# Performance work log

Hardware: AMD Instinct MI355X
Metric: run time of the kernel (lower is better)

The kernel has to match this reference:

```python
import jax, jax.numpy as jnp
import numpy as np

B, C, H, W = 16, 64, 64, 64

def setup_inputs() -> dict:
    key = jax.random.key(0)
    k1, k2, k3, k4, k5 = jax.random.split(key, 5)
    x = jax.random.normal(k1, (B, C, H, W), dtype=jnp.float32)
    w1 = jax.random.normal(k2, (C // 2, C), dtype=jnp.float32) * (1.0 / np.sqrt(C))
    w2 = jax.random.normal(k3, (C // 2, C), dtype=jnp.float32) * (1.0 / np.sqrt(C))
    w3 = jax.random.normal(k4, (C, C), dtype=jnp.float32) * (1.0 / np.sqrt(C))
    gamma = jax.random.normal(k5, (1,), dtype=jnp.float32)
    return {"x": x, "w1": w1, "w2": w2, "w3": w3, "gamma": gamma}

def reference(x, w1, w2, w3, gamma):
    b, c, h, w = x.shape
    n = h * w
    xf = x.reshape(b, c, n)                      # [B, C, N] (1x1 conv == channel matmul)
    c1 = jnp.einsum('dc,bcn->bdn', w1, xf)       # [B, C/2, N]
    c2 = jnp.einsum('dc,bcn->bdn', w2, xf)       # [B, C/2, N]
    c3 = jnp.einsum('oc,bcn->bon', w3, xf)       # [B, C, N]
    # matrix[b,i,j] = sum_d c2[b,d,i] * c1[b,d,j]
    matrix = jnp.einsum('bdi,bdj->bij', c2, c1)  # [B, N, N]
    attention = jax.nn.softmax(matrix, axis=-1)  # softmax over last dim
    # refined[b,c,k] = sum_j c3[b,c,j] * attention[b,k,j]
    refined = jnp.einsum('bcj,bkj->bck', c3, attention)  # [B, C, N]
    refined = refined.reshape(b, c, h, w)
    return gamma[0] * refined + x
```

## Files before the change

kernel.cpp:

```cpp
#include <hip/hip_runtime.h>
#include <hip/hip_bf16.h>

#define Bn 16
#define Nn 4096

typedef __attribute__((ext_vector_type(8))) short bf16x8;
typedef __attribute__((ext_vector_type(16))) float f32x16;

static __device__ __forceinline__ unsigned short f2bf(float f) {
    union { float f; unsigned int u; } v; v.f = f;
    return (unsigned short)((v.u + 0x7fffu + ((v.u >> 16) & 1u)) >> 16);
}
static __device__ __forceinline__ int cvtpk(float lo, float hi) {
    int d; asm("v_cvt_pk_bf16_f32 %0, %1, %2" : "=v"(d) : "v"(lo), "v"(hi)); return d;
}
static __device__ __forceinline__ bf16x8 mkfrag(int a, int b, int c, int d) {
    union { int i[4]; bf16x8 v; } u; u.i[0]=a; u.i[1]=b; u.i[2]=c; u.i[3]=d; return u.v;
}

__global__ __launch_bounds__(256) void qkv_kernel(
    const float* __restrict__ x,
    const float* __restrict__ w1,
    const float* __restrict__ w2,
    const float* __restrict__ w3,
    uint4* __restrict__ Qf,
    uint4* __restrict__ Kf,
    uint4* __restrict__ Vf)
{
    __shared__ float wlds[128 * 64];
    __shared__ __align__(16) unsigned short vtile[64][136];

    const int t = threadIdx.x;
    {
        float4* wd = (float4*)wlds;
        const float4* s1 = (const float4*)w1;
        const float4* s2 = (const float4*)w2;
        const float4* s3 = (const float4*)w3;
        wd[t]       = s1[t];
        wd[256 + t] = s1[256 + t];
        wd[512 + t] = s2[t];
        wd[768 + t] = s2[256 + t];
        #pragma unroll
        for (int k = 0; k < 4; ++k) wd[1024 + k * 256 + t] = s3[k * 256 + t];
    }

    const int half = t >> 7;
    const int nl = t & 127;
    const int b = blockIdx.x >> 5;
    const int n = ((blockIdx.x & 31) << 7) + nl;
    const float* xb = x + ((size_t)b << 18) + n;
    float xr[64];
    #pragma unroll
    for (int c = 0; c < 64; ++c) xr[c] = xb[(size_t)c << 12];

    __syncthreads();

    if (half == 0) {
        const int ntile = ((blockIdx.x & 31) << 2) + (nl >> 5);
        #pragma unroll
        for (int sel = 0; sel < 2; ++sel) {
            const float* wbase = wlds + sel * 2048;
            uint4* dst = (sel ? Qf : Kf) + (((size_t)b * 128 + ntile) * 2) * 64;
            #pragma unroll
            for (int dt = 0; dt < 2; ++dt) {
                float acc[16];
                #pragma unroll
                for (int i = 0; i < 16; ++i) {
                    const float* wr = wbase + (dt * 16 + i) * 64;
                    float a = 0.f;
                    #pragma unroll
                    for (int c4 = 0; c4 < 16; ++c4) {
                        const float4 wv = *(const float4*)(wr + c4 * 4);
                        a = fmaf(wv.x, xr[c4 * 4 + 0], a);
                        a = fmaf(wv.y, xr[c4 * 4 + 1], a);
                        a = fmaf(wv.z, xr[c4 * 4 + 2], a);
                        a = fmaf(wv.w, xr[c4 * 4 + 3], a);
                    }
                    acc[i] = a;
                }
                uint4 u0, u1;
                u0.x = (unsigned)f2bf(acc[0])  | ((unsigned)f2bf(acc[1])  << 16);
                u0.y = (unsigned)f2bf(acc[2])  | ((unsigned)f2bf(acc[3])  << 16);
                u0.z = (unsigned)f2bf(acc[4])  | ((unsigned)f2bf(acc[5])  << 16);
                u0.w = (unsigned)f2bf(acc[6])  | ((unsigned)f2bf(acc[7])  << 16);
                u1.x = (unsigned)f2bf(acc[8])  | ((unsigned)f2bf(acc[9])  << 16);
                u1.y = (unsigned)f2bf(acc[10]) | ((unsigned)f2bf(acc[11]) << 16);
                u1.z = (unsigned)f2bf(acc[12]) | ((unsigned)f2bf(acc[13]) << 16);
                u1.w = (unsigned)f2bf(acc[14]) | ((unsigned)f2bf(acc[15]) << 16);
                dst[(size_t)dt * 64 + (nl & 31)]      = u0;
                dst[(size_t)dt * 64 + 32 + (nl & 31)] = u1;
            }
        }
    } else {
        #pragma unroll
        for (int dg = 0; dg < 8; ++dg) {
            #pragma unroll
            for (int i = 0; i < 8; ++i) {
                const float* wr = wlds + (64 + dg * 8 + i) * 64;
                float a = 0.f;
                #pragma unroll
                for (int c4 = 0; c4 < 16; ++c4) {
                    const float4 wv = *(const float4*)(wr + c4 * 4);
                    a = fmaf(wv.x, xr[c4 * 4 + 0], a);
                    a = fmaf(wv.y, xr[c4 * 4 + 1], a);
                    a = fmaf(wv.z, xr[c4 * 4 + 2], a);
                    a = fmaf(wv.w, xr[c4 * 4 + 3], a);
                }
                vtile[dg * 8 + i][nl] = f2bf(a);
            }
        }
    }
    __syncthreads();

    #pragma unroll
    for (int i = 0; i < 4; ++i) {
        const int slot = t * 4 + i;
        const int l   = slot & 63;
        const int jt  = (slot >> 6) & 1;
        const int ct  = (slot >> 7) & 1;
        const int kvt = slot >> 8;
        const int row  = ct * 32 + (l & 31);
        const int base = kvt * 32 + jt * 16 + ((l >> 5) << 2);
        const uint2 lo = *(const uint2*)&vtile[row][base];
        const uint2 hi = *(const uint2*)&vtile[row][base + 8];
        const int kvtg = ((blockIdx.x & 31) << 2) + kvt;
        Vf[((((size_t)b * 128 + kvtg) * 2 + ct) * 2 + jt) * 64 + l] =
            make_uint4(lo.x, lo.y, hi.x, hi.y);
    }
}

__global__ __launch_bounds__(256) void attn_kernel(
    const bf16x8* __restrict__ Qf,
    const bf16x8* __restrict__ Kf,
    const bf16x8* __restrict__ Vf,
    const float* __restrict__ x,
    const float* __restrict__ gamma,
    float* __restrict__ out)
{
    __shared__ __align__(16) unsigned char kvbuf[2 * 6144];

    const int t    = threadIdx.x;
    const int lane = t & 63;
    const int wv   = t >> 6;
    const int id   = blockIdx.x;
    const int b    = 2 * (id & 7) + ((id >> 3) >> 5);
    const int qblk = (id >> 3) & 31;
    const int qt   = qblk * 4 + wv;

    const bf16x8* Qp = Qf + ((size_t)(b * 128 + qt) * 2) * 64;
    const bf16x8  qf0 = Qp[lane];
    const bf16x8  qf1 = Qp[64 + lane];
    const bf16x8* Kp = Kf + (size_t)b * 128 * 2 * 64;
    const bf16x8* Vp = Vf + (size_t)b * 128 * 4 * 64;

    const int s0i = t >> 6;
    const int l0  = t & 63;
    const bool two = (t < 128);
    const int s1i = 4 + (t >> 6);

    #define SRC_OF(SLOT, NX) ((SLOT) < 2 ? (Kp + ((size_t)(NX) * 2 + (SLOT)) * 64) \
                                         : (Vp + ((size_t)(NX) * 4 + ((SLOT) - 2)) * 64))

    {
        uint4 st0 = *(const uint4*)(SRC_OF(s0i, 0) + l0);
        uint4 st1 = two ? *(const uint4*)(SRC_OF(s1i, 0) + l0) : make_uint4(0, 0, 0, 0);
        *(uint4*)(kvbuf + t * 16) = st0;
        if (two) *(uint4*)(kvbuf + 4096 + t * 16) = st1;
    }
    __syncthreads();

    f32x16 o0 = {}, o1 = {};
    float lacc = 0.f;

    for (int kvt = 0; kvt < 128; ++kvt) {
        uint4 st0, st1;
        if (kvt < 127) {
            st0 = *(const uint4*)(SRC_OF(s0i, kvt + 1) + l0);
            if (two) st1 = *(const uint4*)(SRC_OF(s1i, kvt + 1) + l0);
        }

        const bf16x8* bc = (const bf16x8*)(kvbuf + (kvt & 1) * 6144);
        const bf16x8 kf0 = bc[lane];
        const bf16x8 kf1 = bc[64 + lane];
        const bf16x8 v00 = bc[128 + lane];
        const bf16x8 v01 = bc[192 + lane];
        const bf16x8 v10 = bc[256 + lane];
        const bf16x8 v11 = bc[320 + lane];

        f32x16 s;
        {
            f32x16 z = {};
            s = __builtin_amdgcn_mfma_f32_32x32x16_bf16(kf0, qf0, z, 0, 0, 0);
            s = __builtin_amdgcn_mfma_f32_32x32x16_bf16(kf1, qf1, s, 0, 0, 0);
        }

        float p[16];
        #pragma unroll
        for (int i = 0; i < 16; ++i) p[i] = __expf(s[i]);
        float b0 = (p[0] + p[1]) + (p[2] + p[3]);
        float b1 = (p[4] + p[5]) + (p[6] + p[7]);
        float b2 = (p[8] + p[9]) + (p[10] + p[11]);
        float b3 = (p[12] + p[13]) + (p[14] + p[15]);
        lacc += (b0 + b1) + (b2 + b3);

        const bf16x8 pf0 = mkfrag(cvtpk(p[0],  p[1]),  cvtpk(p[2],  p[3]),
                                  cvtpk(p[4],  p[5]),  cvtpk(p[6],  p[7]));
        const bf16x8 pf1 = mkfrag(cvtpk(p[8],  p[9]),  cvtpk(p[10], p[11]),
                                  cvtpk(p[12], p[13]), cvtpk(p[14], p[15]));

        o0 = __builtin_amdgcn_mfma_f32_32x32x16_bf16(v00, pf0, o0, 0, 0, 0);
        o0 = __builtin_amdgcn_mfma_f32_32x32x16_bf16(v01, pf1, o0, 0, 0, 0);
        o1 = __builtin_amdgcn_mfma_f32_32x32x16_bf16(v10, pf0, o1, 0, 0, 0);
        o1 = __builtin_amdgcn_mfma_f32_32x32x16_bf16(v11, pf1, o1, 0, 0, 0);

        if (kvt < 127) {
            unsigned char* bo = kvbuf + ((kvt + 1) & 1) * 6144;
            *(uint4*)(bo + t * 16) = st0;
            if (two) *(uint4*)(bo + 4096 + t * 16) = st1;
        }
        __syncthreads();
    }
    #undef SRC_OF

    const float g = gamma[0];
    const float lt = lacc + __shfl_xor(lacc, 32, 64);
    const float rl = 1.0f / lt;
    const int n = qt * 32 + (lane & 31);
    const int hi1 = lane >> 5;
    #pragma unroll
    for (int r = 0; r < 16; ++r) {
        const int c0r = (r & 3) + 8 * (r >> 2) + 4 * hi1;
        {
            const size_t idx = (((size_t)b * 64 + c0r) << 12) + n;
            out[idx] = g * o0[r] * rl + x[idx];
        }
        {
            const size_t idx = (((size_t)b * 64 + 32 + c0r) << 12) + n;
            out[idx] = g * o1[r] * rl + x[idx];
        }
    }
}

extern "C" void kernel_launch(void* const* d_in, const int* in_sizes, int n_in,
                              void* d_out, int out_size, void* d_ws, size_t ws_size,
                              hipStream_t stream) {
    const float* x     = (const float*)d_in[0];
    const float* w1    = (const float*)d_in[1];
    const float* w2    = (const float*)d_in[2];
    const float* w3    = (const float*)d_in[3];
    const float* gamma = (const float*)d_in[4];
    float* out = (float*)d_out;

    uint4* Qf = (uint4*)d_ws;
    uint4* Kf = Qf + (size_t)Bn * 128 * 2 * 64;
    uint4* Vf = Kf + (size_t)Bn * 128 * 2 * 64;

    qkv_kernel<<<512, 256, 0, stream>>>(x, w1, w2, w3, Qf, Kf, Vf);
    attn_kernel<<<512, 256, 0, stream>>>((const bf16x8*)Qf, (const bf16x8*)Kf,
                                         (const bf16x8*)Vf, x, gamma, out);
}
```

Measured before the change: 117.9 us.

## Load K/V fragments directly from global into registers, drop LDS staging

Replaces the shared-memory double-buffered K/V staging, and its per-iteration block barrier, with each wave loading its K and V fragments straight from global memory into registers, prefetching the next tile one iteration ahead. This removes the LDS writes and reads and the __syncthreads per KV tile. In exchange, every wave in a block now issues the same global loads independently, roughly four times the global/L2 traffic, and relies on cache hits. Register pressure also rises from holding the prefetched fragments.

Result: slower. 123.9 us (+5.1%).

```diff
diff --git a/kernel.cpp b/kernel.cpp
--- a/kernel.cpp
+++ b/kernel.cpp
@@ -137,8 +137,6 @@
     const float* __restrict__ gamma,
     float* __restrict__ out)
 {
-    __shared__ __align__(16) unsigned char kvbuf[2 * 6144];
-
     const int t    = threadIdx.x;
     const int lane = t & 63;
     const int wv   = t >> 6;
@@ -150,42 +148,24 @@
     const bf16x8* Qp = Qf + ((size_t)(b * 128 + qt) * 2) * 64;
     const bf16x8  qf0 = Qp[lane];
     const bf16x8  qf1 = Qp[64 + lane];
-    const bf16x8* Kp = Kf + (size_t)b * 128 * 2 * 64;
-    const bf16x8* Vp = Vf + (size_t)b * 128 * 4 * 64;
-
-    const int s0i = t >> 6;
-    const int l0  = t & 63;
-    const bool two = (t < 128);
-    const int s1i = 4 + (t >> 6);
-
-    #define SRC_OF(SLOT, NX) ((SLOT) < 2 ? (Kp + ((size_t)(NX) * 2 + (SLOT)) * 64) \
-                                         : (Vp + ((size_t)(NX) * 4 + ((SLOT) - 2)) * 64))
-
-    {
-        uint4 st0 = *(const uint4*)(SRC_OF(s0i, 0) + l0);
-        uint4 st1 = two ? *(const uint4*)(SRC_OF(s1i, 0) + l0) : make_uint4(0, 0, 0, 0);
-        *(uint4*)(kvbuf + t * 16) = st0;
-        if (two) *(uint4*)(kvbuf + 4096 + t * 16) = st1;
-    }
-    __syncthreads();
+    const bf16x8* Kp = Kf + (size_t)b * 128 * 2 * 64 + lane;
+    const bf16x8* Vp = Vf + (size_t)b * 128 * 4 * 64 + lane;
 
     f32x16 o0 = {}, o1 = {};
     float lacc = 0.f;
 
+    bf16x8 kf0 = Kp[0],   kf1 = Kp[64];
+    bf16x8 v00 = Vp[0],   v01 = Vp[64];
+    bf16x8 v10 = Vp[128], v11 = Vp[192];
+
     for (int kvt = 0; kvt < 128; ++kvt) {
-        uint4 st0, st1;
-        if (kvt < 127) {
-            st0 = *(const uint4*)(SRC_OF(s0i, kvt + 1) + l0);
-            if (two) st1 = *(const uint4*)(SRC_OF(s1i, kvt + 1) + l0);
-        }
-
-        const bf16x8* bc = (const bf16x8*)(kvbuf + (kvt & 1) * 6144);
-        const bf16x8 kf0 = bc[lane];
-        const bf16x8 kf1 = bc[64 + lane];
-        const bf16x8 v00 = bc[128 + lane];
-        const bf16x8 v01 = bc[192 + lane];
-        const bf16x8 v10 = bc[256 + lane];
-        const bf16x8 v11 = bc[320 + lane];
+        const int nx = kvt + (kvt < 127);
+        const bf16x8 nk0 = Kp[(size_t)(nx * 2) * 64];
+        const bf16x8 nk1 = Kp[(size_t)(nx * 2 + 1) * 64];
+        const bf16x8 nv00 = Vp[(size_t)(nx * 4) * 64];
+        const bf16x8 nv01 = Vp[(size_t)(nx * 4 + 1) * 64];
+        const bf16x8 nv10 = Vp[(size_t)(nx * 4 + 2) * 64];
+        const bf16x8 nv11 = Vp[(size_t)(nx * 4 + 3) * 64];
 
         f32x16 s;
         {
@@ -213,14 +193,9 @@
         o1 = __builtin_amdgcn_mfma_f32_32x32x16_bf16(v10, pf0, o1, 0, 0, 0);
         o1 = __builtin_amdgcn_mfma_f32_32x32x16_bf16(v11, pf1, o1, 0, 0, 0);
 
-        if (kvt < 127) {
-            unsigned char* bo = kvbuf + ((kvt + 1) & 1) * 6144;
-            *(uint4*)(bo + t * 16) = st0;
-            if (two) *(uint4*)(bo + 4096 + t * 16) = st1;
-        }
-        __syncthreads();
-    }
-    #undef SRC_OF
+        kf0 = nk0; kf1 = nk1;
+        v00 = nv00; v01 = nv01; v10 = nv10; v11 = nv11;
+    }
 
     const float g = gamma[0];
     const float lt = lacc + __shfl_xor(lacc, 32, 64);
```

## Split KV loop across two wave groups per block and merge partials in LDS

Applied to the files above, without the earlier changes.

The attention kernel now launches 512 threads per block. Two halves of 4 waves each process separate halves of the key/value sequence for the same query tiles, which halves the serial loop length from 128 to 64 iterations. The second half writes its partial output accumulators and row sums to shared memory, and the first half adds them before the epilogue. This doubles the waves resident per block to improve latency hiding, at the cost of more LDS, an extra barrier and merge step, and possibly lower occupancy per CU. The merge is valid without a running max because softmax here uses plain exp with no max subtraction.

Result: faster. 109.5 us (-7.2%).

```diff
diff --git a/kernel.cpp b/kernel.cpp
--- a/kernel.cpp
+++ b/kernel.cpp
@@ -129,7 +129,7 @@
     }
 }
 
-__global__ __launch_bounds__(256) void attn_kernel(
+__global__ __launch_bounds__(512) void attn_kernel(
     const bf16x8* __restrict__ Qf,
     const bf16x8* __restrict__ Kf,
     const bf16x8* __restrict__ Vf,
@@ -137,15 +137,17 @@
     const float* __restrict__ gamma,
     float* __restrict__ out)
 {
-    __shared__ __align__(16) unsigned char kvbuf[2 * 6144];
+    __shared__ __align__(16) unsigned char kvbuf[2 * 12288];
+    __shared__ float mgbuf[4 * 64 * 37];
 
     const int t    = threadIdx.x;
     const int lane = t & 63;
     const int wv   = t >> 6;
     const int id   = blockIdx.x;
     const int b    = 2 * (id & 7) + ((id >> 3) >> 5);
-    const int qblk = (id >> 3) & 31;
-    const int qt   = qblk * 4 + wv;
+    const int qg   = (id >> 3) & 31;
+    const int qt   = qg * 4 + (wv & 3);
+    const int h    = wv >> 2;
 
     const bf16x8* Qp = Qf + ((size_t)(b * 128 + qt) * 2) * 64;
     const bf16x8  qf0 = Qp[lane];
@@ -153,33 +155,40 @@
     const bf16x8* Kp = Kf + (size_t)b * 128 * 2 * 64;
     const bf16x8* Vp = Vf + (size_t)b * 128 * 4 * 64;
 
-    const int s0i = t >> 6;
-    const int l0  = t & 63;
-    const bool two = (t < 128);
-    const int s1i = 4 + (t >> 6);
-
-    #define SRC_OF(SLOT, NX) ((SLOT) < 2 ? (Kp + ((size_t)(NX) * 2 + (SLOT)) * 64) \
-                                         : (Vp + ((size_t)(NX) * 4 + ((SLOT) - 2)) * 64))
+    const int s0  = (t >= 384);
+    const int r0  = t - s0 * 384;
+    const int sl0 = r0 >> 6;
+    const int l0  = r0 & 63;
+    const int dof0 = s0 * 12288 + r0 * 16;
+    const bool two = (t < 256);
+    const int r1  = t + 128;
+    const int sl1 = r1 >> 6;
+    const int l1  = t & 63;
+    const int dof1 = 12288 + r1 * 16;
+
+    #define SRC_OF(SLOT, S, NX, LN)                                              \
+        ((SLOT) < 2 ? (Kp + ((size_t)((S) * 64 + (NX)) * 2 + (SLOT)) * 64 + (LN)) \
+                    : (Vp + ((size_t)((S) * 64 + (NX)) * 4 + ((SLOT) - 2)) * 64 + (LN)))
 
     {
-        uint4 st0 = *(const uint4*)(SRC_OF(s0i, 0) + l0);
-        uint4 st1 = two ? *(const uint4*)(SRC_OF(s1i, 0) + l0) : make_uint4(0, 0, 0, 0);
-        *(uint4*)(kvbuf + t * 16) = st0;
-        if (two) *(uint4*)(kvbuf + 4096 + t * 16) = st1;
+        uint4 st0 = *(const uint4*)SRC_OF(sl0, s0, 0, l0);
+        uint4 st1 = two ? *(const uint4*)SRC_OF(sl1, 1, 0, l1) : make_uint4(0, 0, 0, 0);
+        *(uint4*)(kvbuf + dof0) = st0;
+        if (two) *(uint4*)(kvbuf + dof1) = st1;
     }
     __syncthreads();
 
     f32x16 o0 = {}, o1 = {};
     float lacc = 0.f;
 
-    for (int kvt = 0; kvt < 128; ++kvt) {
+    for (int i = 0; i < 64; ++i) {
         uint4 st0, st1;
-        if (kvt < 127) {
-            st0 = *(const uint4*)(SRC_OF(s0i, kvt + 1) + l0);
-            if (two) st1 = *(const uint4*)(SRC_OF(s1i, kvt + 1) + l0);
-        }
-
-        const bf16x8* bc = (const bf16x8*)(kvbuf + (kvt & 1) * 6144);
+        if (i < 63) {
+            st0 = *(const uint4*)SRC_OF(sl0, s0, i + 1, l0);
+            if (two) st1 = *(const uint4*)SRC_OF(sl1, 1, i + 1, l1);
+        }
+
+        const bf16x8* bc = (const bf16x8*)(kvbuf + h * 12288 + (i & 1) * 6144);
         const bf16x8 kf0 = bc[lane];
         const bf16x8 kf1 = bc[64 + lane];
         const bf16x8 v00 = bc[128 + lane];
@@ -196,7 +205,7 @@
 
         float p[16];
         #pragma unroll
-        for (int i = 0; i < 16; ++i) p[i] = __expf(s[i]);
+        for (int j = 0; j < 16; ++j) p[j] = __expf(s[j]);
         float b0 = (p[0] + p[1]) + (p[2] + p[3]);
         float b1 = (p[4] + p[5]) + (p[6] + p[7]);
         float b2 = (p[8] + p[9]) + (p[10] + p[11]);
@@ -213,30 +222,44 @@
         o1 = __builtin_amdgcn_mfma_f32_32x32x16_bf16(v10, pf0, o1, 0, 0, 0);
         o1 = __builtin_amdgcn_mfma_f32_32x32x16_bf16(v11, pf1, o1, 0, 0, 0);
 
-        if (kvt < 127) {
-            unsigned char* bo = kvbuf + ((kvt + 1) & 1) * 6144;
-            *(uint4*)(bo + t * 16) = st0;
-            if (two) *(uint4*)(bo + 4096 + t * 16) = st1;
+        if (i < 63) {
+            const int bo = ((i + 1) & 1) * 6144;
+            *(uint4*)(kvbuf + dof0 + bo) = st0;
+            if (two) *(uint4*)(kvbuf + dof1 + bo) = st1;
         }
         __syncthreads();
     }
     #undef SRC_OF
 
-    const float g = gamma[0];
-    const float lt = lacc + __shfl_xor(lacc, 32, 64);
-    const float rl = 1.0f / lt;
-    const int n = qt * 32 + (lane & 31);
-    const int hi1 = lane >> 5;
-    #pragma unroll
-    for (int r = 0; r < 16; ++r) {
-        const int c0r = (r & 3) + 8 * (r >> 2) + 4 * hi1;
-        {
-            const size_t idx = (((size_t)b * 64 + c0r) << 12) + n;
-            out[idx] = g * o0[r] * rl + x[idx];
-        }
-        {
-            const size_t idx = (((size_t)b * 64 + 32 + c0r) << 12) + n;
-            out[idx] = g * o1[r] * rl + x[idx];
+    if (wv >= 4) {
+        float* mg = mgbuf + ((size_t)(wv - 4) * 64 + lane) * 37;
+        #pragma unroll
+        for (int j = 0; j < 16; ++j) { mg[j] = o0[j]; mg[16 + j] = o1[j]; }
+        mg[32] = lacc;
+    }
+    __syncthreads();
+    if (wv < 4) {
+        const float* mg = mgbuf + ((size_t)wv * 64 + lane) * 37;
+        #pragma unroll
+        for (int j = 0; j < 16; ++j) { o0[j] += mg[j]; o1[j] += mg[16 + j]; }
+        lacc += mg[32];
+
+        const float g = gamma[0];
+        const float lt = lacc + __shfl_xor(lacc, 32, 64);
+        const float rl = 1.0f / lt;
+        const int n = qt * 32 + (lane & 31);
+        const int hi1 = lane >> 5;
+        #pragma unroll
+        for (int r = 0; r < 16; ++r) {
+            const int c0r = (r & 3) + 8 * (r >> 2) + 4 * hi1;
+            {
+                const size_t idx = (((size_t)b * 64 + c0r) << 12) + n;
+                out[idx] = g * o0[r] * rl + x[idx];
+            }
+            {
+                const size_t idx = (((size_t)b * 64 + 32 + c0r) << 12) + n;
+                out[idx] = g * o1[r] * rl + x[idx];
+            }
         }
     }
 }
@@ -256,6 +279,6 @@
     uint4* Vf = Kf + (size_t)Bn * 128 * 2 * 64;
 
     qkv_kernel<<<512, 256, 0, stream>>>(x, w1, w2, w3, Qf, Kf, Vf);
-    attn_kernel<<<512, 256, 0, stream>>>((const bf16x8*)Qf, (const bf16x8*)Kf,
+    attn_kernel<<<512, 512, 0, stream>>>((const bf16x8*)Qf, (const bf16x8*)Kf,
                                          (const bf16x8*)Vf, x, gamma, out);
 }
```
